# Kernel optimization log

Measured on AMD Instinct MI355X. Metric: run time of the kernel, lower is better.

## Reference

```python
import jax, jax.numpy as jnp
from jax import lax
import numpy as np
import math

EPS = 1e-5
NBINS = 17   # quantized color levels round(x*255/16) for x in [0,1)
K_MODE = 11

def _bn(x, g, b):
    # BatchNorm2d in training mode: batch statistics over (B,H,W)
    m = jnp.mean(x, axis=(0, 2, 3), keepdims=True)
    v = jnp.var(x, axis=(0, 2, 3), keepdims=True)
    return (x - m) * lax.rsqrt(v + EPS) * g[None, :, None, None] + b[None, :, None, None]

def _lrelu(x):
    return jnp.where(x >= 0, x, 0.01 * x)

def _shared_conv(x, w, b, stride, padding):
    # one KxK kernel shared depthwise across all channels, scalar bias
    C = x.shape[1]
    k = jnp.tile(w[None, None], (C, 1, 1, 1))  # (C,1,K,K)
    y = lax.conv_general_dilated(x, k, (stride, stride),
                                 [(padding, padding), (padding, padding)],
                                 dimension_numbers=('NCHW', 'OIHW', 'NCHW'),
                                 feature_group_count=C)
    return y + b[0]

def _avg_pool_same(x, k):
    # avg_pool2d(k, stride=1, padding=k//2, count_include_pad=True)
    p = k // 2
    s = lax.reduce_window(x, 0.0, lax.add, (1, 1, k, k), (1, 1, 1, 1),
                          [(0, 0), (0, 0), (p, p), (p, p)])
    return s / float(k * k)

def _mode_pool(xq):
    # xq values are exact multiples of 16/256 -> recover integer bin index,
    # then mode over 11x11 window = argmax of per-bin counts (histogram).
    # torch zero-padding corresponds to bin 0; argmax first-max tie-break ->
    # smallest value, matching torch.mode.
    q = jnp.clip(jnp.round(xq * (256.0 / 16.0)).astype(jnp.int32), 0, NBINS - 1)
    pad = K_MODE // 2
    qp = jnp.pad(q, ((0, 0), (0, 0), (pad, pad), (pad, pad)))
    onehot = (qp[:, :, None] == jnp.arange(NBINS, dtype=jnp.int32)[None, None, :, None, None]).astype(jnp.float32)
    counts = lax.reduce_window(onehot, 0.0, lax.add, (1, 1, 1, K_MODE, K_MODE), (1, 1, 1, 1, 1), 'VALID')
    mode_bin = jnp.argmax(counts, axis=2)  # (B,C,H,W)
    return mode_bin.astype(xq.dtype) * (16.0 / 256.0)

def _forward(x, p_w1, p_b1, p_dw1, p_db1, p_g1, p_be1,
             p_w2, p_b2, p_dw2, p_db2, p_g2, p_be2,
             d_w, d_b, ia_w, ia_b, ia_g, ia_be,
             ib_w, ib_b, ib_g, ib_be,
             f_g1, f_be1, f_g2, f_be2):
    xq = jnp.round(x * (255.0 / 16.0)) * (16.0 / 256.0)
    xm = _mode_pool(xq)
    B, C, H, W = xm.shape
    half = p_w1.shape[0]

    # prepare: 1x1 conv -> depthwise 1x1 (per-channel scale) -> BN -> LeakyReLU, twice
    h = jnp.einsum('bchw,oc->bohw', xm, p_w1) + p_b1[None, :, None, None]
    h = h * p_dw1[None, :, None, None] + p_db1[None, :, None, None]
    h = _lrelu(_bn(h, p_g1, p_be1))
    h = jnp.einsum('bchw,oc->bohw', h, p_w2) + p_b2[None, :, None, None]
    h = h * p_dw2[None, :, None, None] + p_db2[None, :, None, None]
    h = _lrelu(_bn(h, p_g2, p_be2))

    n = int(math.floor(math.log(min(H, W), 3)))
    score = jnp.zeros((B, 2 * half, H, W), x.dtype)
    d = h
    for _ in range(n):
        d = _shared_conv(d, d_w, d_b, 3, 1)  # stride-3 downgrade
        z = jax.image.resize(d, (B, half, H, W), method='bilinear')
        a = _lrelu(_bn(_shared_conv(z, ia_w, ia_b, 1, 2), ia_g, ia_be))
        bb = _lrelu(_bn(_shared_conv(z, ib_w, ib_b, 1, 2), ib_g, ib_be))
        score = score + jnp.concatenate([a, bb], axis=1)  # Splitter + Stack(1)

    def ft(s):
        s = _bn(s, f_g1, f_be1)
        s = jnp.where(s > 0.1, 0.1 + 0.7 * (s - 0.1), s)  # MaxLeakyReLU(0.7, 0.1)
        s = _bn(s, f_g2, f_be2)
        return 2.0 * s - _avg_pool_same(s, K_MODE)  # EmphaseLocal(11): x + (x - local mean)

    score = ft(ft(ft(score)))
    return score / n

def setup_inputs() -> dict:
    key = jax.random.key(0)
    ks = jax.random.split(key, 32)
    B, Cin, H, W, half = 8, 3, 384, 384, 32
    r = lambda i, shp, s=0.1: s * jax.random.normal(ks[i], shp, dtype=jnp.float32)
    g = lambda i, shp: 1.0 + 0.1 * jax.random.normal(ks[i], shp, dtype=jnp.float32)
    return dict(
        x=jax.random.uniform(ks[0], (B, Cin, H, W), dtype=jnp.float32),
        p_w1=r(1, (half, Cin), 0.3), p_b1=r(2, (half,)),
        p_dw1=g(3, (half,)), p_db1=r(4, (half,)),
        p_g1=g(5, (half,)), p_be1=r(6, (half,)),
        p_w2=r(7, (half, half), 0.2), p_b2=r(8, (half,)),
        p_dw2=g(9, (half,)), p_db2=r(10, (half,)),
        p_g2=g(11, (half,)), p_be2=r(12, (half,)),
        d_w=r(13, (3, 3), 0.2), d_b=r(14, (1,)),
        ia_w=r(15, (5, 5), 0.2), ia_b=r(16, (1,)),
        ia_g=g(17, (half,)), ia_be=r(18, (half,)),
        ib_w=r(19, (5, 5), 0.2), ib_b=r(20, (1,)),
        ib_g=g(21, (half,)), ib_be=r(22, (half,)),
        f_g1=g(23, (2 * half,)), f_be1=r(24, (2 * half,)),
        f_g2=g(25, (2 * half,)), f_be2=r(26, (2 * half,)),
    )

def reference(x, p_w1, p_b1, p_dw1, p_db1, p_g1, p_be1,
              p_w2, p_b2, p_dw2, p_db2, p_g2, p_be2,
              d_w, d_b, ia_w, ia_b, ia_g, ia_be,
              ib_w, ib_b, ib_g, ib_be,
              f_g1, f_be1, f_g2, f_be2):
    return _forward(x, p_w1, p_b1, p_dw1, p_db1, p_g1, p_be1,
                    p_w2, p_b2, p_dw2, p_db2, p_g2, p_be2,
                    d_w, d_b, ia_w, ia_b, ia_g, ia_be,
                    ib_w, ib_b, ib_g, ib_be,
                    f_g1, f_be1, f_g2, f_be2)
```

## Files before the change

### kernel.cpp

```cpp
#include <hip/hip_runtime.h>

#define HW 147456
#define WID 384
#define NB 8
#define NPC 1179648
#define HW4 36864
#define ZS 76

static __device__ __forceinline__ float lrelu01(float v) { return v >= 0.f ? v : 0.01f * v; }
static __device__ __forceinline__ float mlrelu(float v) { return v > 0.1f ? 0.1f + 0.7f * (v - 0.1f) : v; }

__global__ __launch_bounds__(256) void mode_kernel(const float* __restrict__ x,
                                                   float* __restrict__ xm) {
  __shared__ unsigned char qt[26 * 76];
  __shared__ unsigned int cc[16 * 5 * 76];
  const int plane = blockIdx.z;
  const int x0 = blockIdx.x * 64;
  const int y0 = blockIdx.y * 16;
  const float* xp = x + (size_t)plane * HW;

  for (int i = threadIdx.x; i < 26 * 76; i += 256) {
    int r = i / 76, ccol = i - r * 76;
    int gy = y0 + r - 5, gx = x0 + ccol - 5;
    unsigned char q = 0;
    if (ccol < 74 && gy >= 0 && gy < WID && gx >= 0 && gx < WID) {
      float v = xp[gy * WID + gx];
      int qi = (int)rintf(v * 15.9375f);
      qi = qi < 0 ? 0 : (qi > 16 ? 16 : qi);
      q = (unsigned char)qi;
    }
    qt[i] = q;
  }
  __syncthreads();

  for (int i = threadIdx.x; i < 16 * 74; i += 256) {
    int yy = i / 74, col = i - yy * 74;
    unsigned int w0 = 0, w1 = 0, w2 = 0, w3 = 0, w4 = 0;
#pragma unroll
    for (int dy = 0; dy < 11; ++dy) {
      int q = qt[(yy + dy) * 76 + col];
      unsigned int inc = 1u << ((q & 3) << 3);
      int wsel = q >> 2;
      w0 += (wsel == 0) ? inc : 0u;
      w1 += (wsel == 1) ? inc : 0u;
      w2 += (wsel == 2) ? inc : 0u;
      w3 += (wsel == 3) ? inc : 0u;
      w4 += (wsel == 4) ? inc : 0u;
    }
    cc[(yy * 5 + 0) * 76 + col] = w0;
    cc[(yy * 5 + 1) * 76 + col] = w1;
    cc[(yy * 5 + 2) * 76 + col] = w2;
    cc[(yy * 5 + 3) * 76 + col] = w3;
    cc[(yy * 5 + 4) * 76 + col] = w4;
  }
  __syncthreads();

  for (int i = threadIdx.x; i < 16 * 64; i += 256) {
    int yy = i / 64, xx = i - yy * 64;
    unsigned int s0 = 0, s1 = 0, s2 = 0, s3 = 0, s4 = 0;
#pragma unroll
    for (int dx = 0; dx < 11; ++dx) {
      int col = xx + dx;
      s0 += cc[(yy * 5 + 0) * 76 + col];
      s1 += cc[(yy * 5 + 1) * 76 + col];
      s2 += cc[(yy * 5 + 2) * 76 + col];
      s3 += cc[(yy * 5 + 3) * 76 + col];
      s4 += cc[(yy * 5 + 4) * 76 + col];
    }
    unsigned int words[5] = {s0, s1, s2, s3, s4};
    int best = 0;
    unsigned int bc = s0 & 0xffu;
#pragma unroll
    for (int bin = 1; bin < 17; ++bin) {
      unsigned int cnt = (words[bin >> 2] >> ((bin & 3) * 8)) & 0xffu;
      if (cnt > bc) { bc = cnt; best = bin; }
    }
    xm[(size_t)plane * HW + (size_t)(y0 + yy) * WID + (x0 + xx)] = best * 0.0625f;
  }
}

__global__ __launch_bounds__(256) void xm_mom(const float4* __restrict__ X,
                                              float* __restrict__ part9) {
  float s0 = 0, s1 = 0, s2 = 0, m00 = 0, m01 = 0, m02 = 0, m11 = 0, m12 = 0, m22 = 0;
  const int end = (blockIdx.x + 1) * 1152;
  for (int u = blockIdx.x * 1152 + threadIdx.x; u < end; u += 256) {
    int b = u / HW4, p4 = u - b * HW4;
    const float4* base = X + (size_t)b * 3 * HW4 + p4;
    float4 a = base[0], bb = base[HW4], c = base[2 * HW4];
    s0 += a.x + a.y + a.z + a.w;
    s1 += bb.x + bb.y + bb.z + bb.w;
    s2 += c.x + c.y + c.z + c.w;
    m00 += a.x * a.x + a.y * a.y + a.z * a.z + a.w * a.w;
    m01 += a.x * bb.x + a.y * bb.y + a.z * bb.z + a.w * bb.w;
    m02 += a.x * c.x + a.y * c.y + a.z * c.z + a.w * c.w;
    m11 += bb.x * bb.x + bb.y * bb.y + bb.z * bb.z + bb.w * bb.w;
    m12 += bb.x * c.x + bb.y * c.y + bb.z * c.z + bb.w * c.w;
    m22 += c.x * c.x + c.y * c.y + c.z * c.z + c.w * c.w;
  }
  float vals[9] = {s0, s1, s2, m00, m01, m02, m11, m12, m22};
  int lane = threadIdx.x & 63, wd = threadIdx.x >> 6;
  __shared__ float red[4][9];
#pragma unroll
  for (int j = 0; j < 9; ++j) {
    float v = vals[j];
    for (int off = 32; off; off >>= 1) v += __shfl_down(v, off);
    if (lane == 0) red[wd][j] = v;
  }
  __syncthreads();
  if (threadIdx.x < 9)
    part9[blockIdx.x * 9 + threadIdx.x] =
        red[0][threadIdx.x] + red[1][threadIdx.x] + red[2][threadIdx.x] + red[3][threadIdx.x];
}

__global__ __launch_bounds__(64) void prep1_affine(const float* __restrict__ part9,
                                                   const float* __restrict__ w1,
                                                   const float* __restrict__ b1,
                                                   const float* __restrict__ dw1,
                                                   const float* __restrict__ db1,
                                                   const float* __restrict__ g,
                                                   const float* __restrict__ be,
                                                   float* __restrict__ sc,
                                                   float* __restrict__ sh) {
  __shared__ double M[9];
  if (threadIdx.x < 9) {
    double s = 0.0;
    for (int i = 0; i < 256; ++i) s += (double)part9[i * 9 + threadIdx.x];
    M[threadIdx.x] = s;
  }
  __syncthreads();
  if (threadIdx.x < 32) {
    int o = threadIdx.x;
    double dw = dw1[o];
    double a0 = (double)w1[o * 3] * dw, a1 = (double)w1[o * 3 + 1] * dw,
           a2 = (double)w1[o * 3 + 2] * dw;
    double k = (double)b1[o] * dw + (double)db1[o];
    double N = (double)NPC;
    double lin = (a0 * M[0] + a1 * M[1] + a2 * M[2]) / N;
    double mean = lin + k;
    double e2 = (a0 * a0 * M[3] + a1 * a1 * M[6] + a2 * a2 * M[8] +
                 2.0 * (a0 * a1 * M[4] + a0 * a2 * M[5] + a1 * a2 * M[7])) / N +
                2.0 * k * lin + k * k;
    double var = e2 - mean * mean;
    float rstd = rsqrtf((float)var + 1e-5f);
    float scl = rstd * g[o];
    sc[o] = scl;
    sh[o] = be[o] - (float)mean * scl;
  }
}

__global__ __launch_bounds__(256) void prep_fused(const float* __restrict__ xm,
                                                  const float* __restrict__ w1,
                                                  const float* __restrict__ b1,
                                                  const float* __restrict__ dw1,
                                                  const float* __restrict__ db1,
                                                  const float* __restrict__ P1SC,
                                                  const float* __restrict__ P1SH,
                                                  const float* __restrict__ w2,
                                                  const float* __restrict__ b2,
                                                  const float* __restrict__ dw2,
                                                  const float* __restrict__ db2,
                                                  float* __restrict__ t2,
                                                  float* __restrict__ part) {
  __shared__ float wl[1024];
  __shared__ float c1[32][4];
  __shared__ float bias2[32];
  __shared__ float wred[8][32];
  for (int i = threadIdx.x; i < 1024; i += 256) wl[i] = w2[i] * dw2[i >> 5];
  if (threadIdx.x < 32) {
    int o = threadIdx.x;
    float dw = dw1[o], s1 = P1SC[o];
    c1[o][0] = w1[o * 3] * dw * s1;
    c1[o][1] = w1[o * 3 + 1] * dw * s1;
    c1[o][2] = w1[o * 3 + 2] * dw * s1;
    c1[o][3] = (b1[o] * dw + db1[o]) * s1 + P1SH[o];
    bias2[o] = b2[o] * dw2[o] + db2[o];
  }
  __syncthreads();
  const int p0 = blockIdx.x * 512 + threadIdx.x;
  const int b = p0 / HW, pp = p0 - b * HW;
  const float* xb = xm + (size_t)b * 3 * HW + pp;
  float h[2][32];
#pragma unroll
  for (int q = 0; q < 2; ++q) {
    float x0 = xb[q * 256], x1 = xb[HW + q * 256], x2 = xb[2 * HW + q * 256];
#pragma unroll
    for (int o = 0; o < 32; ++o) {
      float u = fmaf(x0, c1[o][0], fmaf(x1, c1[o][1], fmaf(x2, c1[o][2], c1[o][3])));
      h[q][o] = lrelu01(u);
    }
  }
  float sv[32], sq[32];
  float* ob = t2 + (size_t)b * 32 * HW + pp;
  const float4* wl4 = reinterpret_cast<const float4*>(wl);
  for (int o = 0; o < 32; ++o) {
    float acc0 = bias2[o], acc1 = bias2[o];
#pragma unroll
    for (int c4 = 0; c4 < 8; ++c4) {
      float4 w4 = wl4[o * 8 + c4];
      int c = c4 * 4;
      acc0 = fmaf(h[0][c], w4.x, acc0);     acc1 = fmaf(h[1][c], w4.x, acc1);
      acc0 = fmaf(h[0][c + 1], w4.y, acc0); acc1 = fmaf(h[1][c + 1], w4.y, acc1);
      acc0 = fmaf(h[0][c + 2], w4.z, acc0); acc1 = fmaf(h[1][c + 2], w4.z, acc1);
      acc0 = fmaf(h[0][c + 3], w4.w, acc0); acc1 = fmaf(h[1][c + 3], w4.w, acc1);
    }
    ob[(size_t)o * HW] = acc0;
    ob[(size_t)o * HW + 256] = acc1;
    sv[o] = acc0 + acc1;
    sq[o] = acc0 * acc0 + acc1 * acc1;
  }
  int lane = threadIdx.x & 63, wd = threadIdx.x >> 6;
#pragma unroll
  for (int o = 0; o < 32; ++o) {
    float a = sv[o], q = sq[o];
    for (int off = 32; off; off >>= 1) {
      a += __shfl_down(a, off);
      q += __shfl_down(q, off);
    }
    if (lane == 0) { wred[wd][o] = a; wred[wd + 4][o] = q; }
  }
  __syncthreads();
  if (threadIdx.x < 32) {
    int o = threadIdx.x;
    part[((size_t)o * 2304 + blockIdx.x) * 2] = wred[0][o] + wred[1][o] + wred[2][o] + wred[3][o];
    part[((size_t)o * 2304 + blockIdx.x) * 2 + 1] = wred[4][o] + wred[5][o] + wred[6][o] + wred[7][o];
  }
}

__global__ __launch_bounds__(64) void stats_combine(const float* __restrict__ part, int nsplit,
                                                    const float* __restrict__ g,
                                                    const float* __restrict__ be,
                                                    float* __restrict__ sc,
                                                    float* __restrict__ sh) {
  const int c = blockIdx.x;
  double s = 0.0, q = 0.0;
  for (int i = threadIdx.x; i < nsplit; i += 64) {
    s += part[((size_t)c * nsplit + i) * 2];
    q += part[((size_t)c * nsplit + i) * 2 + 1];
  }
  for (int off = 32; off; off >>= 1) {
    s += __shfl_down(s, off);
    q += __shfl_down(q, off);
  }
  if (threadIdx.x == 0) {
    double mean = s / (double)NPC;
    double var = q / (double)NPC - mean * mean;
    float rstd = rsqrtf((float)var + 1e-5f);
    float scl = rstd * g[c];
    sc[c] = scl;
    sh[c] = be[c] - (float)mean * scl;
  }
}

template <bool AFF>
__global__ __launch_bounds__(256) void dconv(const float* __restrict__ in,
                                             const float* __restrict__ sc,
                                             const float* __restrict__ sh,
                                             const float* __restrict__ w9,
                                             const float* __restrict__ db,
                                             int Sin, int Sout,
                                             float* __restrict__ out, int total) {
  int idx = blockIdx.x * 256 + threadIdx.x;
  if (idx >= total) return;
  int xx = idx % Sout;
  int t = idx / Sout;
  int yy = t % Sout;
  int pc = t / Sout;
  int c = pc & 31;
  const float* ip = in + (size_t)pc * Sin * Sin;
  float a = AFF ? sc[c] : 1.f;
  float h = AFF ? sh[c] : 0.f;
  float acc = 0.f;
#pragma unroll
  for (int ky = 0; ky < 3; ++ky) {
    int iy = 3 * yy - 1 + ky;
    if (iy < 0 || iy >= Sin) continue;
#pragma unroll
    for (int kx = 0; kx < 3; ++kx) {
      int ix = 3 * xx - 1 + kx;
      if (ix < 0 || ix >= Sin) continue;
      float v = ip[(size_t)iy * Sin + ix];
      if (AFF) { v = v * a + h; v = lrelu01(v); }
      acc = fmaf(v, w9[ky * 3 + kx], acc);
    }
  }
  out[idx] = acc + db[0];
}

static __device__ __forceinline__ int sin_of(int l) {
  return l == 0 ? 128 : l == 1 ? 43 : l == 2 ? 15 : l == 3 ? 5 : 2;
}

__global__ __launch_bounds__(256) void geo_build(float4* __restrict__ geo) {
  int id = blockIdx.x * 256 + threadIdx.x;
  if (id >= 5 * 384) return;
  int l = id / 384, p = id - l * 384;
  int Sin = sin_of(l);
  float scale = (float)Sin / 384.f;
  float s = (p + 0.5f) * scale - 0.5f;
  float f0 = floorf(s);
  float fr = s - f0;
  int ii = (int)f0;
  int i1 = ii + 1 < Sin - 1 ? ii + 1 : Sin - 1;
  int i0 = ii > 0 ? ii : 0;
  geo[id] = make_float4((float)i0, (float)i1, fr, 0.f);
}

static __device__ __forceinline__ int clamp383(int v) {
  return v < 0 ? 0 : (v > 383 ? 383 : v);
}

__device__ __forceinline__ void conv2row(const float* zt, int u, int g,
                                         const float* wa, const float* wb,
                                         float ba0, float bb0,
                                         float* A0, float* A1, float* B0, float* B1) {
#pragma unroll
  for (int j = 0; j < 4; ++j) { A0[j] = ba0; A1[j] = ba0; B0[j] = bb0; B1[j] = bb0; }
  const float* zp = zt + (2 * u) * ZS + g * 4;
#pragma unroll
  for (int zr = 0; zr < 6; ++zr) {
    float4 zlo = *reinterpret_cast<const float4*>(zp + zr * ZS);
    float4 zhi = *reinterpret_cast<const float4*>(zp + zr * ZS + 4);
    float z[8] = {zlo.x, zlo.y, zlo.z, zlo.w, zhi.x, zhi.y, zhi.z, zhi.w};
    if (zr < 5) {
#pragma unroll
      for (int dx = 0; dx < 5; ++dx) {
        float wva = wa[zr * 5 + dx], wvb = wb[zr * 5 + dx];
#pragma unroll
        for (int j = 0; j < 4; ++j) {
          A0[j] = fmaf(z[dx + j], wva, A0[j]);
          B0[j] = fmaf(z[dx + j], wvb, B0[j]);
        }
      }
    }
    if (zr >= 1) {
#pragma unroll
      for (int dx = 0; dx < 5; ++dx) {
        float wva = wa[(zr - 1) * 5 + dx], wvb = wb[(zr - 1) * 5 + dx];
#pragma unroll
        for (int j = 0; j < 4; ++j) {
          A1[j] = fmaf(z[dx + j], wva, A1[j]);
          B1[j] = fmaf(z[dx + j], wvb, B1[j]);
        }
      }
    }
  }
}

__global__ __launch_bounds__(256) void upstats64(const float* __restrict__ d1,
                                                 const float* __restrict__ d2,
                                                 const float* __restrict__ d3,
                                                 const float* __restrict__ d4,
                                                 const float* __restrict__ d5,
                                                 const float4* __restrict__ geo,
                                                 const float* __restrict__ wA5,
                                                 const float* __restrict__ wB5,
                                                 const float* __restrict__ bA,
                                                 const float* __restrict__ bB,
                                                 float* __restrict__ partA,
                                                 float* __restrict__ partB) {
  __shared__ __align__(16) float zt[2][36 * ZS];
  __shared__ __align__(16) float dH[2][16 * ZS];
  __shared__ float red[2][16];
  const int lvl = blockIdx.z;
  const float* dsel = lvl == 0 ? d1 : lvl == 1 ? d2 : lvl == 2 ? d3 : lvl == 3 ? d4 : d5;
  const int Sin = sin_of(lvl);
  const int plane0 = blockIdx.y * 2, tile = blockIdx.x;
  const int tx = (tile % 6) * 64, ty = (tile / 6) * 32;
  const float4* xg = geo + lvl * 384;
  const float* dp0 = dsel + (size_t)plane0 * Sin * Sin;
  const float* dp1 = dp0 + Sin * Sin;

  float wa[25], wb[25];
#pragma unroll
  for (int k = 0; k < 25; ++k) { wa[k] = wA5[k]; wb[k] = wB5[k]; }
  const float ba0 = bA[0], bb0 = bB[0];

  const int rowlo = (int)xg[clamp383(ty - 2)].x;
  const int rowhi = (int)xg[clamp383(ty + 33)].y;
  const int nr = rowhi - rowlo + 1;
  const int cnt = nr * 68;

  for (int i = threadIdx.x; i < 2 * cnt; i += 256) {
    int p = i < cnt ? 0 : 1;
    int j = i - p * cnt;
    int r = j / 68, zx = j - r * 68;
    int gp = tx + zx - 2;
    int gpc = clamp383(gp);
    float vd = (gp == gpc) ? 1.f : 0.f;
    float4 ge = xg[gpc];
    const float* drow = (p ? dp1 : dp0) + (size_t)(rowlo + r) * Sin;
    float v0 = drow[(int)ge.x], v1 = drow[(int)ge.y];
    dH[p][r * ZS + zx] = (v0 + ge.z * (v1 - v0)) * vd;
  }
  __syncthreads();
  for (int i = threadIdx.x; i < 2 * 612; i += 256) {
    int p = i < 612 ? 0 : 1;
    int j = i - p * 612;
    int zy = j / 17, k = j - zy * 17;
    int gp = ty + zy - 2;
    int gpc = clamp383(gp);
    float vd = (gp == gpc) ? 1.f : 0.f;
    float4 ge = xg[gpc];
    int r0 = (int)ge.x - rowlo, r1 = (int)ge.y - rowlo;
    float fy = ge.z;
    float4 a4 = *reinterpret_cast<const float4*>(&dH[p][r0 * ZS + k * 4]);
    float4 b4 = *reinterpret_cast<const float4*>(&dH[p][r1 * ZS + k * 4]);
    float4 o;
    o.x = (a4.x + fy * (b4.x - a4.x)) * vd;
    o.y = (a4.y + fy * (b4.y - a4.y)) * vd;
    o.z = (a4.z + fy * (b4.z - a4.z)) * vd;
    o.w = (a4.w + fy * (b4.w - a4.w)) * vd;
    *reinterpret_cast<float4*>(&zt[p][zy * ZS + k * 4]) = o;
  }
  __syncthreads();

  const int u = threadIdx.x >> 4, g = threadIdx.x & 15;
  const int lane = threadIdx.x & 63, wd = threadIdx.x >> 6;
#pragma unroll
  for (int p = 0; p < 2; ++p) {
    float A0[4], A1[4], B0[4], B1[4];
    conv2row(zt[p], u, g, wa, wb, ba0, bb0, A0, A1, B0, B1);
    float sa = 0.f, qa = 0.f, sb = 0.f, qb = 0.f;
#pragma unroll
    for (int j = 0; j < 4; ++j) {
      sa += A0[j] + A1[j];
      qa += A0[j] * A0[j] + A1[j] * A1[j];
      sb += B0[j] + B1[j];
      qb += B0[j] * B0[j] + B1[j] * B1[j];
    }
    for (int off = 32; off; off >>= 1) {
      sa += __shfl_down(sa, off); qa += __shfl_down(qa, off);
      sb += __shfl_down(sb, off); qb += __shfl_down(qb, off);
    }
    if (lane == 0) {
      red[p][wd * 4 + 0] = sa; red[p][wd * 4 + 1] = qa;
      red[p][wd * 4 + 2] = sb; red[p][wd * 4 + 3] = qb;
    }
  }
  __syncthreads();
  if (threadIdx.x < 2) {
    int p = threadIdx.x;
    int plane = plane0 + p;
    int b = plane >> 5, c = plane & 31;
    const float* r_ = red[p];
    size_t pi = ((size_t)lvl * 32 + c) * 576 * 2 + ((size_t)b * 72 + tile) * 2;
    partA[pi] = r_[0] + r_[4] + r_[8] + r_[12];
    partA[pi + 1] = r_[1] + r_[5] + r_[9] + r_[13];
    partB[pi] = r_[2] + r_[6] + r_[10] + r_[14];
    partB[pi + 1] = r_[3] + r_[7] + r_[11] + r_[15];
  }
}

__global__ __launch_bounds__(64) void combine_lvls(const float* __restrict__ partA,
                                                   const float* __restrict__ partB,
                                                   const float* __restrict__ ia_g,
                                                   const float* __restrict__ ia_be,
                                                   const float* __restrict__ ib_g,
                                                   const float* __restrict__ ib_be,
                                                   float* __restrict__ aff) {
  const int c = blockIdx.x, lvl = blockIdx.y, z = blockIdx.z;
  const float* part = (z ? partB : partA) + (size_t)lvl * 32 * 576 * 2;
  const float* g = z ? ib_g : ia_g;
  const float* be = z ? ib_be : ia_be;
  double s = 0.0, q = 0.0;
  for (int i = threadIdx.x; i < 576; i += 64) {
    s += part[((size_t)c * 576 + i) * 2];
    q += part[((size_t)c * 576 + i) * 2 + 1];
  }
  for (int off = 32; off; off >>= 1) {
    s += __shfl_down(s, off);
    q += __shfl_down(q, off);
  }
  if (threadIdx.x == 0) {
    double mean = s / (double)NPC;
    double var = q / (double)NPC - mean * mean;
    float rstd = rsqrtf((float)var + 1e-5f);
    float scl = rstd * g[c];
    aff[((z * 5 + lvl) * 2 + 0) * 32 + c] = scl;
    aff[((z * 5 + lvl) * 2 + 1) * 32 + c] = be[c] - (float)mean * scl;
  }
}

__global__ __launch_bounds__(256) void apply64(const float* __restrict__ d1,
                                               const float* __restrict__ d2,
                                               const float* __restrict__ d3,
                                               const float* __restrict__ d4,
                                               const float* __restrict__ d5,
                                               const float4* __restrict__ geo,
                                               const float* __restrict__ wA5,
                                               const float* __restrict__ wB5,
                                               const float* __restrict__ bA,
                                               const float* __restrict__ bB,
                                               const float* __restrict__ aff,
                                               float* __restrict__ outp,
                                               float* __restrict__ partF) {
  __shared__ __align__(16) float zt[36 * ZS];
  __shared__ __align__(16) float dH[16 * ZS];
  __shared__ float red[16];
  const int plane = blockIdx.y, tile = blockIdx.x;
  const int tx = (tile % 6) * 64, ty = (tile / 6) * 32;
  const int b = plane >> 5, c = plane & 31;
  float wa[25], wb[25];
#pragma unroll
  for (int k = 0; k < 25; ++k) { wa[k] = wA5[k]; wb[k] = wB5[k]; }
  const float ba0 = bA[0], bb0 = bB[0];
  const int u = threadIdx.x >> 4, g = threadIdx.x & 15;

  float acA0[4] = {0, 0, 0, 0}, acA1[4] = {0, 0, 0, 0};
  float acB0[4] = {0, 0, 0, 0}, acB1[4] = {0, 0, 0, 0};

  for (int l = 0; l < 5; ++l) {
    const float* dsel = l == 0 ? d1 : l == 1 ? d2 : l == 2 ? d3 : l == 3 ? d4 : d5;
    const int Sin = sin_of(l);
    const float* dp = dsel + (size_t)plane * Sin * Sin;
    const float4* xg = geo + l * 384;
    const int rowlo = (int)xg[clamp383(ty - 2)].x;
    const int rowhi = (int)xg[clamp383(ty + 33)].y;
    const int nr = rowhi - rowlo + 1;
    for (int i = threadIdx.x; i < nr * 68; i += 256) {
      int r = i / 68, zx = i - r * 68;
      int gp = tx + zx - 2;
      int gpc = clamp383(gp);
      float vd = (gp == gpc) ? 1.f : 0.f;
      float4 ge = xg[gpc];
      const float* drow = dp + (size_t)(rowlo + r) * Sin;
      float v0 = drow[(int)ge.x], v1 = drow[(int)ge.y];
      dH[r * ZS + zx] = (v0 + ge.z * (v1 - v0)) * vd;
    }
    __syncthreads();
    for (int i = threadIdx.x; i < 612; i += 256) {
      int zy = i / 17, k = i - zy * 17;
      int gp = ty + zy - 2;
      int gpc = clamp383(gp);
      float vd = (gp == gpc) ? 1.f : 0.f;
      float4 ge = xg[gpc];
      int r0 = (int)ge.x - rowlo, r1 = (int)ge.y - rowlo;
      float fy = ge.z;
      float4 a4 = *reinterpret_cast<const float4*>(&dH[r0 * ZS + k * 4]);
      float4 b4 = *reinterpret_cast<const float4*>(&dH[r1 * ZS + k * 4]);
      float4 o;
      o.x = (a4.x + fy * (b4.x - a4.x)) * vd;
      o.y = (a4.y + fy * (b4.y - a4.y)) * vd;
      o.z = (a4.z + fy * (b4.z - a4.z)) * vd;
      o.w = (a4.w + fy * (b4.w - a4.w)) * vd;
      *reinterpret_cast<float4*>(&zt[zy * ZS + k * 4]) = o;
    }
    __syncthreads();
    float A0[4], A1[4], B0[4], B1[4];
    conv2row(zt, u, g, wa, wb, ba0, bb0, A0, A1, B0, B1);
    float as = aff[(l * 2 + 0) * 32 + c], ah = aff[(l * 2 + 1) * 32 + c];
    float bs = aff[((5 + l) * 2 + 0) * 32 + c], bh = aff[((5 + l) * 2 + 1) * 32 + c];
#pragma unroll
    for (int j = 0; j < 4; ++j) {
      acA0[j] += lrelu01(fmaf(A0[j], as, ah));
      acA1[j] += lrelu01(fmaf(A1[j], as, ah));
      acB0[j] += lrelu01(fmaf(B0[j], bs, bh));
      acB1[j] += lrelu01(fmaf(B1[j], bs, bh));
    }
  }

  float4 xa0 = {acA0[0], acA0[1], acA0[2], acA0[3]};
  float4 xa1 = {acA1[0], acA1[1], acA1[2], acA1[3]};
  float4 xb0 = {acB0[0], acB0[1], acB0[2], acB0[3]};
  float4 xb1 = {acB1[0], acB1[1], acB1[2], acB1[3]};
  size_t po = (size_t)(b * 64 + c) * HW + (size_t)(ty + 2 * u) * WID + tx + g * 4;
  *reinterpret_cast<float4*>(outp + po) = xa0;
  *reinterpret_cast<float4*>(outp + po + WID) = xa1;
  *reinterpret_cast<float4*>(outp + po + (size_t)32 * HW) = xb0;
  *reinterpret_cast<float4*>(outp + po + (size_t)32 * HW + WID) = xb1;

  float sa = 0.f, qa = 0.f, sb = 0.f, qb = 0.f;
#pragma unroll
  for (int j = 0; j < 4; ++j) {
    sa += acA0[j] + acA1[j];
    qa += acA0[j] * acA0[j] + acA1[j] * acA1[j];
    sb += acB0[j] + acB1[j];
    qb += acB0[j] * acB0[j] + acB1[j] * acB1[j];
  }
  int lane = threadIdx.x & 63, wd = threadIdx.x >> 6;
  for (int off = 32; off; off >>= 1) {
    sa += __shfl_down(sa, off); qa += __shfl_down(qa, off);
    sb += __shfl_down(sb, off); qb += __shfl_down(qb, off);
  }
  if (lane == 0) {
    red[wd * 4 + 0] = sa; red[wd * 4 + 1] = qa;
    red[wd * 4 + 2] = sb; red[wd * 4 + 3] = qb;
  }
  __syncthreads();
  if (threadIdx.x == 0) {
    size_t piA = ((size_t)c * 576 + (size_t)b * 72 + tile) * 2;
    size_t piB = ((size_t)(c + 32) * 576 + (size_t)b * 72 + tile) * 2;
    partF[piA] = red[0] + red[4] + red[8] + red[12];
    partF[piA + 1] = red[1] + red[5] + red[9] + red[13];
    partF[piB] = red[2] + red[6] + red[10] + red[14];
    partF[piB + 1] = red[3] + red[7] + red[11] + red[15];
  }
}

__global__ __launch_bounds__(256) void stats_mlrelu(const float4* __restrict__ X,
                                                    const float* __restrict__ sc1,
                                                    const float* __restrict__ sh1,
                                                    float* __restrict__ part) {
  int c = blockIdx.x >> 6, s = blockIdx.x & 63;
  float a1 = sc1[c], b1 = sh1[c];
  float sum = 0.f, sq = 0.f;
  int b = s >> 3;
  const float4* Xp = X + (size_t)(b * 64 + c) * HW4 + (s & 7) * 4608 + threadIdx.x;
#pragma unroll 6
  for (int it = 0; it < 18; ++it) {
    float4 v = Xp[it * 256];
    float u;
    u = mlrelu(fmaf(v.x, a1, b1)); sum += u; sq += u * u;
    u = mlrelu(fmaf(v.y, a1, b1)); sum += u; sq += u * u;
    u = mlrelu(fmaf(v.z, a1, b1)); sum += u; sq += u * u;
    u = mlrelu(fmaf(v.w, a1, b1)); sum += u; sq += u * u;
  }
  int lane = threadIdx.x & 63, wd = threadIdx.x >> 6;
  for (int off = 32; off; off >>= 1) {
    sum += __shfl_down(sum, off);
    sq += __shfl_down(sq, off);
  }
  __shared__ float red[8];
  if (lane == 0) { red[wd * 2] = sum; red[wd * 2 + 1] = sq; }
  __syncthreads();
  if (threadIdx.x == 0) {
    part[((size_t)c * 64 + s) * 2] = red[0] + red[2] + red[4] + red[6];
    part[((size_t)c * 64 + s) * 2 + 1] = red[1] + red[3] + red[5] + red[7];
  }
}

__global__ __launch_bounds__(256) void ft_fused(const float* __restrict__ src,
                                                const float* __restrict__ F1SC,
                                                const float* __restrict__ F1SH,
                                                const float* __restrict__ F2SC,
                                                const float* __restrict__ F2SH,
                                                float* __restrict__ dst, float fscale,
                                                float* __restrict__ part) {
  __shared__ float sl[74 * 81];
  __shared__ __align__(16) float Hl[74 * 64];
  __shared__ float red[8];
  const int tile = blockIdx.x;
  const int plane = blockIdx.y;
  const int b = plane >> 6, c = plane & 63;
  const int tx = (tile % 6) * 64, ty = (tile / 6) * 64;
  const float a1 = F1SC[c], b1 = F1SH[c], a2 = F2SC[c], b2 = F2SH[c];
  const float* sp = src + (size_t)plane * HW;

  for (int i = threadIdx.x; i < 74 * 20; i += 256) {
    int r = i / 20, k = i - r * 20;
    int gy = ty + r - 5, gx = tx + k * 4 - 8;
    float4 sv = {0.f, 0.f, 0.f, 0.f};
    if (gy >= 0 && gy < WID && gx >= 0 && gx < WID) {
      float4 v = *reinterpret_cast<const float4*>(sp + (size_t)gy * WID + gx);
      sv.x = fmaf(mlrelu(fmaf(v.x, a1, b1)), a2, b2);
      sv.y = fmaf(mlrelu(fmaf(v.y, a1, b1)), a2, b2);
      sv.z = fmaf(mlrelu(fmaf(v.z, a1, b1)), a2, b2);
      sv.w = fmaf(mlrelu(fmaf(v.w, a1, b1)), a2, b2);
    }
    int base = r * 81 + k * 4;
    sl[base] = sv.x; sl[base + 1] = sv.y; sl[base + 2] = sv.z; sl[base + 3] = sv.w;
  }
  __syncthreads();

  float4* H4 = reinterpret_cast<float4*>(Hl);
  for (int i = threadIdx.x; i < 74 * 16; i += 256) {
    int r = i >> 4, g = i & 15;
    const float* s0 = &sl[r * 81 + g * 4 + 3];
    float v[14];
#pragma unroll
    for (int j = 0; j < 14; ++j) v[j] = s0[j];
    float h0 = v[0] + v[1] + v[2] + v[3] + v[4] + v[5] + v[6] + v[7] + v[8] + v[9] + v[10];
    float h1 = h0 - v[0] + v[11];
    float h2 = h1 - v[1] + v[12];
    float h3 = h2 - v[2] + v[13];
    float4 hh = {h0, h1, h2, h3};
    H4[r * 16 + (g ^ ((r >> 2) & 3))] = hh;
  }
  __syncthreads();

  const int g = threadIdx.x & 15, ly = threadIdx.x >> 4;
  const int y0 = ly * 4;
  float4 acc = H4[y0 * 16 + (g ^ ((y0 >> 2) & 3))];
#pragma unroll
  for (int dy = 1; dy < 11; ++dy) {
    int y = y0 + dy;
    float4 t = H4[y * 16 + (g ^ ((y >> 2) & 3))];
    acc.x += t.x; acc.y += t.y; acc.z += t.z; acc.w += t.w;
  }
  float sum = 0.f, sq = 0.f;
  float* dpo = dst + (size_t)plane * HW;
#pragma unroll
  for (int ry = 0; ry < 4; ++ry) {
    int y = y0 + ry;
    if (ry) {
      int ya = y + 10, yb = y - 1;
      float4 ta = H4[ya * 16 + (g ^ ((ya >> 2) & 3))];
      float4 tb = H4[yb * 16 + (g ^ ((yb >> 2) & 3))];
      acc.x += ta.x - tb.x; acc.y += ta.y - tb.y;
      acc.z += ta.z - tb.z; acc.w += ta.w - tb.w;
    }
    const float* cp = &sl[(y + 5) * 81 + g * 4 + 8];
    float4 o;
    o.x = (2.f * cp[0] - acc.x * (1.f / 121.f)) * fscale;
    o.y = (2.f * cp[1] - acc.y * (1.f / 121.f)) * fscale;
    o.z = (2.f * cp[2] - acc.z * (1.f / 121.f)) * fscale;
    o.w = (2.f * cp[3] - acc.w * (1.f / 121.f)) * fscale;
    *reinterpret_cast<float4*>(dpo + (size_t)(ty + y) * WID + tx + g * 4) = o;
    sum += o.x + o.y + o.z + o.w;
    sq += o.x * o.x + o.y * o.y + o.z * o.z + o.w * o.w;
  }
  if (part) {
    int lane = threadIdx.x & 63, wd = threadIdx.x >> 6;
    for (int off = 32; off; off >>= 1) {
      sum += __shfl_down(sum, off);
      sq += __shfl_down(sq, off);
    }
    if (lane == 0) { red[wd * 2] = sum; red[wd * 2 + 1] = sq; }
    __syncthreads();
    if (threadIdx.x == 0) {
      size_t pi = ((size_t)c * 288 + (size_t)b * 36 + tile) * 2;
      part[pi] = red[0] + red[2] + red[4] + red[6];
      part[pi + 1] = red[1] + red[3] + red[5] + red[7];
    }
  }
}

extern "C" void kernel_launch(void* const* d_in, const int* in_sizes, int n_in,
                              void* d_out, int out_size, void* d_ws, size_t ws_size,
                              hipStream_t stream) {
  const float* x     = (const float*)d_in[0];
  const float* p_w1  = (const float*)d_in[1];
  const float* p_b1  = (const float*)d_in[2];
  const float* p_dw1 = (const float*)d_in[3];
  const float* p_db1 = (const float*)d_in[4];
  const float* p_g1  = (const float*)d_in[5];
  const float* p_be1 = (const float*)d_in[6];
  const float* p_w2  = (const float*)d_in[7];
  const float* p_b2  = (const float*)d_in[8];
  const float* p_dw2 = (const float*)d_in[9];
  const float* p_db2 = (const float*)d_in[10];
  const float* p_g2  = (const float*)d_in[11];
  const float* p_be2 = (const float*)d_in[12];
  const float* d_w   = (const float*)d_in[13];
  const float* d_b   = (const float*)d_in[14];
  const float* ia_w  = (const float*)d_in[15];
  const float* ia_b  = (const float*)d_in[16];
  const float* ia_g  = (const float*)d_in[17];
  const float* ia_be = (const float*)d_in[18];
  const float* ib_w  = (const float*)d_in[19];
  const float* ib_b  = (const float*)d_in[20];
  const float* ib_g  = (const float*)d_in[21];
  const float* ib_be = (const float*)d_in[22];
  const float* f_g1  = (const float*)d_in[23];
  const float* f_be1 = (const float*)d_in[24];
  const float* f_g2  = (const float*)d_in[25];
  const float* f_be2 = (const float*)d_in[26];
  float* out = (float*)d_out;
  float* ws = (float*)d_ws;

  const size_t SLOT = 37748736ull;
  float* B0 = ws;
  float* B1 = ws + 2 * SLOT;
  float* t2 = B0;
  float* partA = B0 + SLOT;
  float* partB = partA + 368640;
  float* partP = partB + 368640;
  float* part9 = partP + 147456;
  float* aff   = part9 + 2304;
  float* xm  = B1;
  float* dd1 = xm + 3538944;
  float* dd2 = dd1 + 4194304;
  float* dd3 = dd2 + 473344;
  float* dd4 = dd3 + 57600;
  float* dd5 = dd4 + 6400;
  float* partF = ws + 4 * SLOT;
  float* partS = partF + 147456;
  float* st    = partS + 8192;
  float* geoT  = st + 512;

  float* P1SC = st,       *P1SH = st + 32;
  float* P2SC = st + 64,  *P2SH = st + 96;
  float* F1SC = st + 128, *F1SH = st + 192;
  float* F2SC = st + 256, *F2SH = st + 320;

  geo_build<<<8, 256, 0, stream>>>((float4*)geoT);
  mode_kernel<<<dim3(6, 24, 24), 256, 0, stream>>>(x, xm);
  xm_mom<<<256, 256, 0, stream>>>((const float4*)xm, part9);
  prep1_affine<<<1, 64, 0, stream>>>(part9, p_w1, p_b1, p_dw1, p_db1, p_g1, p_be1, P1SC, P1SH);
  prep_fused<<<2304, 256, 0, stream>>>(xm, p_w1, p_b1, p_dw1, p_db1, P1SC, P1SH,
                                       p_w2, p_b2, p_dw2, p_db2, t2, partP);
  stats_combine<<<32, 64, 0, stream>>>(partP, 2304, p_g2, p_be2, P2SC, P2SH);

  dconv<true><<<16384, 256, 0, stream>>>(t2, P2SC, P2SH, d_w, d_b, 384, 128, dd1,
                                         8 * 32 * 128 * 128);
  dconv<false><<<(8 * 32 * 43 * 43 + 255) / 256, 256, 0, stream>>>(
      dd1, nullptr, nullptr, d_w, d_b, 128, 43, dd2, 8 * 32 * 43 * 43);
  dconv<false><<<(8 * 32 * 15 * 15 + 255) / 256, 256, 0, stream>>>(
      dd2, nullptr, nullptr, d_w, d_b, 43, 15, dd3, 8 * 32 * 15 * 15);
  dconv<false><<<(8 * 32 * 5 * 5 + 255) / 256, 256, 0, stream>>>(
      dd3, nullptr, nullptr, d_w, d_b, 15, 5, dd4, 8 * 32 * 5 * 5);
  dconv<false><<<(8 * 32 * 2 * 2 + 255) / 256, 256, 0, stream>>>(
      dd4, nullptr, nullptr, d_w, d_b, 5, 2, dd5, 8 * 32 * 2 * 2);

  upstats64<<<dim3(72, 128, 5), 256, 0, stream>>>(dd1, dd2, dd3, dd4, dd5,
                                                  (const float4*)geoT,
                                                  ia_w, ib_w, ia_b, ib_b, partA, partB);
  combine_lvls<<<dim3(32, 5, 2), 64, 0, stream>>>(partA, partB, ia_g, ia_be, ib_g, ib_be, aff);
  apply64<<<dim3(72, 256), 256, 0, stream>>>(dd1, dd2, dd3, dd4, dd5,
                                             (const float4*)geoT,
                                             ia_w, ib_w, ia_b, ib_b, aff, out, partF);

  const float* cur = out;
  float* dsts[3] = {B0, B1, out};
  for (int k = 0; k < 3; ++k) {
    stats_combine<<<64, 64, 0, stream>>>(partF, (k == 0) ? 576 : 288, f_g1, f_be1, F1SC, F1SH);
    stats_mlrelu<<<64 * 64, 256, 0, stream>>>((const float4*)cur, F1SC, F1SH, partS);
    stats_combine<<<64, 64, 0, stream>>>(partS, 64, f_g2, f_be2, F2SC, F2SH);
    ft_fused<<<dim3(36, 512), 256, 0, stream>>>(cur, F1SC, F1SH, F2SC, F2SH, dsts[k],
                                                (k == 2) ? 0.2f : 1.0f,
                                                (k < 2) ? partF : nullptr);
    cur = dsts[k];
  }
}
```

Before: 1.820 ms.

## Enlarge upsample-conv tiles to 64x64 with four output rows per thread

The upstats64 and apply64 kernels now use 64x64 output tiles instead of 64x32, and each thread computes a 4x4 block of the 5x5 convolution instead of 2x4. This cuts the halo overhead of the staged bilinear-upsampled tile (68 rows staged for 64 outputs instead of 36 for 32) and the number of shared-memory row loads per output. The partial-stat buffers shrink to 288 entries per channel. In exchange, each thread holds more accumulators, which raises register pressure, and the larger shared tile may lower occupancy.

```diff
diff --git a/kernel.cpp b/kernel.cpp
--- a/kernel.cpp
+++ b/kernel.cpp
@@ -309,40 +309,68 @@
   return v < 0 ? 0 : (v > 383 ? 383 : v);
 }
 
-__device__ __forceinline__ void conv2row(const float* zt, int u, int g,
+__device__ __forceinline__ void conv4row(const float* zt, int u, int g,
                                          const float* wa, const float* wb,
                                          float ba0, float bb0,
-                                         float* A0, float* A1, float* B0, float* B1) {
-#pragma unroll
-  for (int j = 0; j < 4; ++j) { A0[j] = ba0; A1[j] = ba0; B0[j] = bb0; B1[j] = bb0; }
-  const float* zp = zt + (2 * u) * ZS + g * 4;
-#pragma unroll
-  for (int zr = 0; zr < 6; ++zr) {
+                                         float A[4][4], float Bv[4][4]) {
+#pragma unroll
+  for (int j = 0; j < 4; ++j)
+#pragma unroll
+    for (int p = 0; p < 4; ++p) { A[j][p] = ba0; Bv[j][p] = bb0; }
+  const float* zp = zt + (4 * u) * ZS + g * 4;
+#pragma unroll
+  for (int zr = 0; zr < 8; ++zr) {
     float4 zlo = *reinterpret_cast<const float4*>(zp + zr * ZS);
     float4 zhi = *reinterpret_cast<const float4*>(zp + zr * ZS + 4);
     float z[8] = {zlo.x, zlo.y, zlo.z, zlo.w, zhi.x, zhi.y, zhi.z, zhi.w};
-    if (zr < 5) {
-#pragma unroll
-      for (int dx = 0; dx < 5; ++dx) {
-        float wva = wa[zr * 5 + dx], wvb = wb[zr * 5 + dx];
-#pragma unroll
-        for (int j = 0; j < 4; ++j) {
-          A0[j] = fmaf(z[dx + j], wva, A0[j]);
-          B0[j] = fmaf(z[dx + j], wvb, B0[j]);
+#pragma unroll
+    for (int j = 0; j < 4; ++j) {
+      int dy = zr - j;
+      if (dy >= 0 && dy <= 4) {
+#pragma unroll
+        for (int dx = 0; dx < 5; ++dx) {
+          float wva = wa[dy * 5 + dx], wvb = wb[dy * 5 + dx];
+#pragma unroll
+          for (int p = 0; p < 4; ++p) {
+            A[j][p] = fmaf(z[dx + p], wva, A[j][p]);
+            Bv[j][p] = fmaf(z[dx + p], wvb, Bv[j][p]);
+          }
         }
       }
     }
-    if (zr >= 1) {
-#pragma unroll
-      for (int dx = 0; dx < 5; ++dx) {
-        float wva = wa[(zr - 1) * 5 + dx], wvb = wb[(zr - 1) * 5 + dx];
-#pragma unroll
-        for (int j = 0; j < 4; ++j) {
-          A1[j] = fmaf(z[dx + j], wva, A1[j]);
-          B1[j] = fmaf(z[dx + j], wvb, B1[j]);
-        }
-      }
-    }
+  }
+}
+
+__device__ __forceinline__ void stage64(float* zt, float* dH, const float* dp, int Sin,
+                                        const float4* xg, int tx, int ty,
+                                        int rowlo, int nr) {
+  for (int i = threadIdx.x; i < nr * 68; i += 256) {
+    int r = i / 68, zx = i - r * 68;
+    int gp = tx + zx - 2;
+    int gpc = clamp383(gp);
+    float vd = (gp == gpc) ? 1.f : 0.f;
+    float4 ge = xg[gpc];
+    const float* drow = dp + (size_t)(rowlo + r) * Sin;
+    float v0 = drow[(int)ge.x], v1 = drow[(int)ge.y];
+    dH[r * ZS + zx] = (v0 + ge.z * (v1 - v0)) * vd;
+  }
+  __syncthreads();
+  for (int i = threadIdx.x; i < 68 * 17; i += 256) {
+    int zy = i / 17, k = i - zy * 17;
+    int gp = ty + zy - 2;
+    int gpc = clamp383(gp);
+    float vd = (gp == gpc) ? 1.f : 0.f;
+    float4 ge = xg[gpc];
+    int r0 = (int)ge.x - rowlo, r1 = (int)ge.y - rowlo;
+    float fy = ge.z;
+    float4 a4 = *reinterpret_cast<const float4*>(&dH[r0 * ZS + k * 4]);
+    float4 b4 = *reinterpret_cast<const float4*>(&dH[r1 * ZS + k * 4]);
+    float4 o;
+    o.x = (a4.x + fy * (b4.x - a4.x)) * vd;
+    o.y = (a4.y + fy * (b4.y - a4.y)) * vd;
+    o.z = (a4.z + fy * (b4.z - a4.z)) * vd;
+    o.w = (a4.w + fy * (b4.w - a4.w)) * vd;
+    *reinterpret_cast<float4*>(&zt[zy * ZS + k * 4]) = o;
   }
 }
 
@@ -358,17 +386,16 @@
                                                  const float* __restrict__ bB,
                                                  float* __restrict__ partA,
                                                  float* __restrict__ partB) {
-  __shared__ __align__(16) float zt[2][36 * ZS];
-  __shared__ __align__(16) float dH[2][16 * ZS];
-  __shared__ float red[2][16];
+  __shared__ __align__(16) float zt[68 * ZS];
+  __shared__ __align__(16) float dH[26 * ZS];
+  __shared__ float red[16];
   const int lvl = blockIdx.z;
   const float* dsel = lvl == 0 ? d1 : lvl == 1 ? d2 : lvl == 2 ? d3 : lvl == 3 ? d4 : d5;
   const int Sin = sin_of(lvl);
-  const int plane0 = blockIdx.y * 2, tile = blockIdx.x;
-  const int tx = (tile % 6) * 64, ty = (tile / 6) * 32;
+  const int plane = blockIdx.y, tile = blockIdx.x;
+  const int tx = (tile % 6) * 64, ty = (tile / 6) * 64;
   const float4* xg = geo + lvl * 384;
-  const float* dp0 = dsel + (size_t)plane0 * Sin * Sin;
-  const float* dp1 = dp0 + Sin * Sin;
+  const float* dp = dsel + (size_t)plane * Sin * Sin;
 
   float wa[25], wb[25];
 #pragma unroll
@@ -376,78 +403,40 @@
   const float ba0 = bA[0], bb0 = bB[0];
 
   const int rowlo = (int)xg[clamp383(ty - 2)].x;
-  const int rowhi = (int)xg[clamp383(ty + 33)].y;
+  const int rowhi = (int)xg[clamp383(ty + 65)].y;
   const int nr = rowhi - rowlo + 1;
-  const int cnt = nr * 68;
-
-  for (int i = threadIdx.x; i < 2 * cnt; i += 256) {
-    int p = i < cnt ? 0 : 1;
-    int j = i - p * cnt;
-    int r = j / 68, zx = j - r * 68;
-    int gp = tx + zx - 2;
-    int gpc = clamp383(gp);
-    float vd = (gp == gpc) ? 1.f : 0.f;
-    float4 ge = xg[gpc];
-    const float* drow = (p ? dp1 : dp0) + (size_t)(rowlo + r) * Sin;
-    float v0 = drow[(int)ge.x], v1 = drow[(int)ge.y];
-    dH[p][r * ZS + zx] = (v0 + ge.z * (v1 - v0)) * vd;
-  }
-  __syncthreads();
-  for (int i = threadIdx.x; i < 2 * 612; i += 256) {
-    int p = i < 612 ? 0 : 1;
-    int j = i - p * 612;
-    int zy = j / 17, k = j - zy * 17;
-    int gp = ty + zy - 2;
-    int gpc = clamp383(gp);
-    float vd = (gp == gpc) ? 1.f : 0.f;
-    float4 ge = xg[gpc];
-    int r0 = (int)ge.x - rowlo, r1 = (int)ge.y - rowlo;
-    float fy = ge.z;
-    float4 a4 = *reinterpret_cast<const float4*>(&dH[p][r0 * ZS + k * 4]);
-    float4 b4 = *reinterpret_cast<const float4*>(&dH[p][r1 * ZS + k * 4]);
-    float4 o;
-    o.x = (a4.x + fy * (b4.x - a4.x)) * vd;
-    o.y = (a4.y + fy * (b4.y - a4.y)) * vd;
-    o.z = (a4.z + fy * (b4.z - a4.z)) * vd;
-    o.w = (a4.w + fy * (b4.w - a4.w)) * vd;
-    *reinterpret_cast<float4*>(&zt[p][zy * ZS + k * 4]) = o;
-  }
+
+  stage64(zt, dH, dp, Sin, xg, tx, ty, rowlo, nr);
   __syncthreads();
 
   const int u = threadIdx.x >> 4, g = threadIdx.x & 15;
-  const int lane = threadIdx.x & 63, wd = threadIdx.x >> 6;
-#pragma unroll
-  for (int p = 0; p < 2; ++p) {
-    float A0[4], A1[4], B0[4], B1[4];
-    conv2row(zt[p], u, g, wa, wb, ba0, bb0, A0, A1, B0, B1);
-    float sa = 0.f, qa = 0.f, sb = 0.f, qb = 0.f;
-#pragma unroll
-    for (int j = 0; j < 4; ++j) {
-      sa += A0[j] + A1[j];
-      qa += A0[j] * A0[j] + A1[j] * A1[j];
-      sb += B0[j] + B1[j];
-      qb += B0[j] * B0[j] + B1[j] * B1[j];
-    }
-    for (int off = 32; off; off >>= 1) {
-      sa += __shfl_down(sa, off); qa += __shfl_down(qa, off);
-      sb += __shfl_down(sb, off); qb += __shfl_down(qb, off);
-    }
-    if (lane == 0) {
-      red[p][wd * 4 + 0] = sa; red[p][wd * 4 + 1] = qa;
-      red[p][wd * 4 + 2] = sb; red[p][wd * 4 + 3] = qb;
-    }
-  }
-  __syncthreads();
-  if (threadIdx.x < 2) {
-    int p = threadIdx.x;
-    int plane = plane0 + p;
+  float A[4][4], Bv[4][4];
+  conv4row(zt, u, g, wa, wb, ba0, bb0, A, Bv);
+  float sa = 0.f, qa = 0.f, sb = 0.f, qb = 0.f;
+#pragma unroll
+  for (int j = 0; j < 4; ++j)
+#pragma unroll
+    for (int p = 0; p < 4; ++p) {
+      sa += A[j][p]; qa += A[j][p] * A[j][p];
+      sb += Bv[j][p]; qb += Bv[j][p] * Bv[j][p];
+    }
+  int lane = threadIdx.x & 63, wd = threadIdx.x >> 6;
+  for (int off = 32; off; off >>= 1) {
+    sa += __shfl_down(sa, off); qa += __shfl_down(qa, off);
+    sb += __shfl_down(sb, off); qb += __shfl_down(qb, off);
+  }
+  if (lane == 0) {
+    red[wd * 4 + 0] = sa; red[wd * 4 + 1] = qa;
+    red[wd * 4 + 2] = sb; red[wd * 4 + 3] = qb;
+  }
+  __syncthreads();
+  if (threadIdx.x == 0) {
     int b = plane >> 5, c = plane & 31;
-    const float* r_ = red[p];
-    size_t pi = ((size_t)lvl * 32 + c) * 576 * 2 + ((size_t)b * 72 + tile) * 2;
-    partA[pi] = r_[0] + r_[4] + r_[8] + r_[12];
-    partA[pi + 1] = r_[1] + r_[5] + r_[9] + r_[13];
-    partB[pi] = r_[2] + r_[6] + r_[10] + r_[14];
-    partB[pi + 1] = r_[3] + r_[7] + r_[11] + r_[15];
+    size_t pi = ((size_t)lvl * 32 + c) * 288 * 2 + ((size_t)b * 36 + tile) * 2;
+    partA[pi] = red[0] + red[4] + red[8] + red[12];
+    partA[pi + 1] = red[1] + red[5] + red[9] + red[13];
+    partB[pi] = red[2] + red[6] + red[10] + red[14];
+    partB[pi + 1] = red[3] + red[7] + red[11] + red[15];
   }
 }
 
@@ -459,13 +448,13 @@
                                                    const float* __restrict__ ib_be,
                                                    float* __restrict__ aff) {
   const int c = blockIdx.x, lvl = blockIdx.y, z = blockIdx.z;
-  const float* part = (z ? partB : partA) + (size_t)lvl * 32 * 576 * 2;
+  const float* part = (z ? partB : partA) + (size_t)lvl * 32 * 288 * 2;
   const float* g = z ? ib_g : ia_g;
   const float* be = z ? ib_be : ia_be;
   double s = 0.0, q = 0.0;
-  for (int i = threadIdx.x; i < 576; i += 64) {
-    s += part[((size_t)c * 576 + i) * 2];
-    q += part[((size_t)c * 576 + i) * 2 + 1];
+  for (int i = threadIdx.x; i < 288; i += 64) {
+    s += part[((size_t)c * 288 + i) * 2];
+    q += part[((size_t)c * 288 + i) * 2 + 1];
   }
   for (int off = 32; off; off >>= 1) {
     s += __shfl_down(s, off);
@@ -494,11 +483,11 @@
                                                const float* __restrict__ aff,
                                                float* __restrict__ outp,
                                                float* __restrict__ partF) {
-  __shared__ __align__(16) float zt[36 * ZS];
-  __shared__ __align__(16) float dH[16 * ZS];
+  __shared__ __align__(16) float zt[68 * ZS];
+  __shared__ __align__(16) float dH[26 * ZS];
   __shared__ float red[16];
   const int plane = blockIdx.y, tile = blockIdx.x;
-  const int tx = (tile % 6) * 64, ty = (tile / 6) * 32;
+  const int tx = (tile % 6) * 64, ty = (tile / 6) * 64;
   const int b = plane >> 5, c = plane & 31;
   float wa[25], wb[25];
 #pragma unroll
@@ -506,8 +495,11 @@
   const float ba0 = bA[0], bb0 = bB[0];
   const int u = threadIdx.x >> 4, g = threadIdx.x & 15;
 
-  float acA0[4] = {0, 0, 0, 0}, acA1[4] = {0, 0, 0, 0};
-  float acB0[4] = {0, 0, 0, 0}, acB1[4] = {0, 0, 0, 0};
+  float acA[4][4], acB[4][4];
+#pragma unroll
+  for (int j = 0; j < 4; ++j)
+#pragma unroll
+    for (int p = 0; p < 4; ++p) { acA[j][p] = 0.f; acB[j][p] = 0.f; }
 
   for (int l = 0; l < 5; ++l) {
     const float* dsel = l == 0 ? d1 : l == 1 ? d2 : l == 2 ? d3 : l == 3 ? d4 : d5;
@@ -515,67 +507,37 @@
     const float* dp = dsel + (size_t)plane * Sin * Sin;
     const float4* xg = geo + l * 384;
     const int rowlo = (int)xg[clamp383(ty - 2)].x;
-    const int rowhi = (int)xg[clamp383(ty + 33)].y;
+    const int rowhi = (int)xg[clamp383(ty + 65)].y;
     const int nr = rowhi - rowlo + 1;
-    for (int i = threadIdx.x; i < nr * 68; i += 256) {
-      int r = i / 68, zx = i - r * 68;
-      int gp = tx + zx - 2;
-      int gpc = clamp383(gp);
-      float vd = (gp == gpc) ? 1.f : 0.f;
-      float4 ge = xg[gpc];
-      const float* drow = dp + (size_t)(rowlo + r) * Sin;
-      float v0 = drow[(int)ge.x], v1 = drow[(int)ge.y];
-      dH[r * ZS + zx] = (v0 + ge.z * (v1 - v0)) * vd;
-    }
+    stage64(zt, dH, dp, Sin, xg, tx, ty, rowlo, nr);
     __syncthreads();
-    for (int i = threadIdx.x; i < 612; i += 256) {
-      int zy = i / 17, k = i - zy * 17;
-      int gp = ty + zy - 2;
-      int gpc = clamp383(gp);
-      float vd = (gp == gpc) ? 1.f : 0.f;
-      float4 ge = xg[gpc];
-      int r0 = (int)ge.x - rowlo, r1 = (int)ge.y - rowlo;
-      float fy = ge.z;
-      float4 a4 = *reinterpret_cast<const float4*>(&dH[r0 * ZS + k * 4]);
-      float4 b4 = *reinterpret_cast<const float4*>(&dH[r1 * ZS + k * 4]);
-      float4 o;
-      o.x = (a4.x + fy * (b4.x - a4.x)) * vd;
-      o.y = (a4.y + fy * (b4.y - a4.y)) * vd;
-      o.z = (a4.z + fy * (b4.z - a4.z)) * vd;
-      o.w = (a4.w + fy * (b4.w - a4.w)) * vd;
-      *reinterpret_cast<float4*>(&zt[zy * ZS + k * 4]) = o;
-    }
-    __syncthreads();
-    float A0[4], A1[4], B0[4], B1[4];
-    conv2row(zt, u, g, wa, wb, ba0, bb0, A0, A1, B0, B1);
+    float A[4][4], Bv[4][4];
+    conv4row(zt, u, g, wa, wb, ba0, bb0, A, Bv);
     float as = aff[(l * 2 + 0) * 32 + c], ah = aff[(l * 2 + 1) * 32 + c];
     float bs = aff[((5 + l) * 2 + 0) * 32 + c], bh = aff[((5 + l) * 2 + 1) * 32 + c];
 #pragma unroll
-    for (int j = 0; j < 4; ++j) {
-      acA0[j] += lrelu01(fmaf(A0[j], as, ah));
-      acA1[j] += lrelu01(fmaf(A1[j], as, ah));
-      acB0[j] += lrelu01(fmaf(B0[j], bs, bh));
-      acB1[j] += lrelu01(fmaf(B1[j], bs, bh));
-    }
-  }
-
-  float4 xa0 = {acA0[0], acA0[1], acA0[2], acA0[3]};
-  float4 xa1 = {acA1[0], acA1[1], acA1[2], acA1[3]};
-  float4 xb0 = {acB0[0], acB0[1], acB0[2], acB0[3]};
-  float4 xb1 = {acB1[0], acB1[1], acB1[2], acB1[3]};
-  size_t po = (size_t)(b * 64 + c) * HW + (size_t)(ty + 2 * u) * WID + tx + g * 4;
-  *reinterpret_cast<float4*>(outp + po) = xa0;
-  *reinterpret_cast<float4*>(outp + po + WID) = xa1;
-  *reinterpret_cast<float4*>(outp + po + (size_t)32 * HW) = xb0;
-  *reinterpret_cast<float4*>(outp + po + (size_t)32 * HW + WID) = xb1;
-
+    for (int j = 0; j < 4; ++j)
+#pragma unroll
+      for (int p = 0; p < 4; ++p) {
+        acA[j][p] += lrelu01(fmaf(A[j][p], as, ah));
+        acB[j][p] += lrelu01(fmaf(Bv[j][p], bs, bh));
+      }
+    __syncthreads();
+  }
+
+  size_t po = (size_t)(b * 64 + c) * HW + (size_t)(ty + 4 * u) * WID + tx + g * 4;
   float sa = 0.f, qa = 0.f, sb = 0.f, qb = 0.f;
 #pragma unroll
   for (int j = 0; j < 4; ++j) {
-    sa += acA0[j] + acA1[j];
-    qa += acA0[j] * acA0[j] + acA1[j] * acA1[j];
-    sb += acB0[j] + acB1[j];
-    qb += acB0[j] * acB0[j] + acB1[j] * acB1[j];
+    float4 xa = {acA[j][0], acA[j][1], acA[j][2], acA[j][3]};
+    float4 xb = {acB[j][0], acB[j][1], acB[j][2], acB[j][3]};
+    *reinterpret_cast<float4*>(outp + po + (size_t)j * WID) = xa;
+    *reinterpret_cast<float4*>(outp + po + (size_t)32 * HW + (size_t)j * WID) = xb;
+#pragma unroll
+    for (int p = 0; p < 4; ++p) {
+      sa += acA[j][p]; qa += acA[j][p] * acA[j][p];
+      sb += acB[j][p]; qb += acB[j][p] * acB[j][p];
+    }
   }
   int lane = threadIdx.x & 63, wd = threadIdx.x >> 6;
   for (int off = 32; off; off >>= 1) {
@@ -588,8 +550,8 @@
   }
   __syncthreads();
   if (threadIdx.x == 0) {
-    size_t piA = ((size_t)c * 576 + (size_t)b * 72 + tile) * 2;
-    size_t piB = ((size_t)(c + 32) * 576 + (size_t)b * 72 + tile) * 2;
+    size_t piA = ((size_t)c * 288 + (size_t)b * 36 + tile) * 2;
+    size_t piB = ((size_t)(c + 32) * 288 + (size_t)b * 36 + tile) * 2;
     partF[piA] = red[0] + red[4] + red[8] + red[12];
     partF[piA + 1] = red[1] + red[5] + red[9] + red[13];
     partF[piB] = red[2] + red[6] + red[10] + red[14];
@@ -802,18 +764,18 @@
   dconv<false><<<(8 * 32 * 2 * 2 + 255) / 256, 256, 0, stream>>>(
       dd4, nullptr, nullptr, d_w, d_b, 5, 2, dd5, 8 * 32 * 2 * 2);
 
-  upstats64<<<dim3(72, 128, 5), 256, 0, stream>>>(dd1, dd2, dd3, dd4, dd5,
+  upstats64<<<dim3(36, 256, 5), 256, 0, stream>>>(dd1, dd2, dd3, dd4, dd5,
                                                   (const float4*)geoT,
                                                   ia_w, ib_w, ia_b, ib_b, partA, partB);
   combine_lvls<<<dim3(32, 5, 2), 64, 0, stream>>>(partA, partB, ia_g, ia_be, ib_g, ib_be, aff);
-  apply64<<<dim3(72, 256), 256, 0, stream>>>(dd1, dd2, dd3, dd4, dd5,
+  apply64<<<dim3(36, 256), 256, 0, stream>>>(dd1, dd2, dd3, dd4, dd5,
                                              (const float4*)geoT,
                                              ia_w, ib_w, ia_b, ib_b, aff, out, partF);
 
   const float* cur = out;
   float* dsts[3] = {B0, B1, out};
   for (int k = 0; k < 3; ++k) {
-    stats_combine<<<64, 64, 0, stream>>>(partF, (k == 0) ? 576 : 288, f_g1, f_be1, F1SC, F1SH);
+    stats_combine<<<64, 64, 0, stream>>>(partF, 288, f_g1, f_be1, F1SC, F1SH);
     stats_mlrelu<<<64 * 64, 256, 0, stream>>>((const float4*)cur, F1SC, F1SH, partS);
     stats_combine<<<64, 64, 0, stream>>>(partS, 64, f_g2, f_be2, F2SC, F2SH);
     ft_fused<<<dim3(36, 512), 256, 0, stream>>>(cur, F1SC, F1SH, F2SC, F2SH, dsts[k],
```

After: 1.731 ms (median of 2 runs). -4.9%, faster.
